# Kernel tuning notes

Hardware: AMD Instinct MI355X
Metric: run time of the kernel (lower is better)

## Reference

```python
import jax, jax.numpy as jnp
import numpy as np

HEADS = 4
SPARSITY_WEIGHT = 0.1
LN_EPS = 1e-5


def setup_inputs() -> dict:
    key = jax.random.key(0)
    ks = jax.random.split(key, 6)
    b, n, d = 4, 2048, 512
    x = jax.random.normal(ks[0], (b, n, d), dtype=jnp.float32)
    alibi_bias = jax.random.normal(ks[1], (b, n, n), dtype=jnp.float32)
    gamma = jax.random.normal(ks[2], (b, d), dtype=jnp.float32)
    beta = jax.random.normal(ks[3], (b, d), dtype=jnp.float32)
    ln_w = jnp.ones((d,), dtype=jnp.float32)
    ln_b = jnp.zeros((d,), dtype=jnp.float32)
    w_qkv = jax.random.normal(ks[4], (d, 3 * d), dtype=jnp.float32) * (d ** -0.5)
    w_out = jax.random.normal(ks[5], (d, d), dtype=jnp.float32) * (d ** -0.5)
    return {"x": x, "alibi_bias": alibi_bias, "gamma": gamma, "beta": beta,
            "ln_w": ln_w, "ln_b": ln_b, "w_qkv": w_qkv, "w_out": w_out}


def reference(x, alibi_bias, gamma, beta, ln_w, ln_b, w_qkv, w_out):
    b, n, d = x.shape
    dh = d // HEADS
    scale = dh ** -0.5
    # LayerNorm over last dim
    mu = jnp.mean(x, axis=-1, keepdims=True)
    var = jnp.mean(jnp.square(x - mu), axis=-1, keepdims=True)
    xn = (x - mu) * jax.lax.rsqrt(var + LN_EPS) * ln_w + ln_b
    # FiLM
    xn = gamma[:, None, :] * xn + beta[:, None, :]
    # QKV projection (Linear, no bias)
    qkv = xn @ w_qkv  # [b, n, 3d]
    q, k, v = jnp.split(qkv, 3, axis=-1)
    split_heads = lambda t: t.reshape(b, n, HEADS, dh).transpose(0, 2, 1, 3)  # b h n d
    q, k, v = split_heads(q), split_heads(k), split_heads(v)
    dots = jnp.einsum('bhid,bhjd->bhij', q, k) * scale
    dots = dots + alibi_bias[:, None, :, :]  # broadcast over heads
    attn = jax.nn.softmax(dots, axis=-1)
    eps = 1e-8
    entropy = -(attn * jnp.log(attn + eps)).sum(axis=-1)
    sparsity_loss = entropy.mean() * SPARSITY_WEIGHT
    out = jnp.einsum('bhij,bhjd->bhid', attn, v)
    out = out.transpose(0, 2, 1, 3).reshape(b, n, d)
    return out @ w_out, sparsity_loss
```

## Files before the change

### kernel.cpp

```cpp
#include <hip/hip_runtime.h>
#include <hip/hip_bf16.h>

typedef __attribute__((ext_vector_type(8))) short short8;
typedef __attribute__((ext_vector_type(4))) short short4_t;
typedef __attribute__((ext_vector_type(4))) float f32x4;

static constexpr int NN = 2048, DD = 512;
static constexpr float SCALE = 0.088388347648318447f;
static constexpr float ENT_SCALE = 0.1f / 32768.0f;

__device__ __forceinline__ short f2bf(float f) {
  __hip_bfloat16 h = __float2bfloat16(f);
  return *reinterpret_cast<short*>(&h);
}

__device__ __forceinline__ void async_cp16(const void* g, void* l) {
  __builtin_amdgcn_global_load_lds((const __attribute__((address_space(1))) void*)g,
                                   (__attribute__((address_space(3))) void*)l, 16, 0, 0);
}

__global__ __launch_bounds__(256) void ln_film_k(
    const float* __restrict__ x, const float* __restrict__ gamma,
    const float* __restrict__ beta, const float* __restrict__ lnw,
    const float* __restrict__ lnb, short* __restrict__ xn) {
  const int wave = threadIdx.x >> 6, lane = threadIdx.x & 63;
  const int row = blockIdx.x * 4 + wave;
  const int b = row >> 11;
  const float4* xr = reinterpret_cast<const float4*>(x + (size_t)row * DD);
  float4 u = xr[lane * 2], v = xr[lane * 2 + 1];
  float s  = u.x + u.y + u.z + u.w + v.x + v.y + v.z + v.w;
  float ss = u.x*u.x + u.y*u.y + u.z*u.z + u.w*u.w + v.x*v.x + v.y*v.y + v.z*v.z + v.w*v.w;
  #pragma unroll
  for (int m = 1; m < 64; m <<= 1) { s += __shfl_xor(s, m); ss += __shfl_xor(ss, m); }
  const float mu = s * (1.0f / DD);
  const float rs = rsqrtf(ss * (1.0f / DD) - mu * mu + 1e-5f);
  const int c0 = lane * 8;
  float vals[8] = {u.x,u.y,u.z,u.w,v.x,v.y,v.z,v.w};
  short8 o;
  #pragma unroll
  for (int i = 0; i < 8; ++i) {
    const int c = c0 + i;
    const float t = (vals[i] - mu) * rs * lnw[c] + lnb[c];
    o[i] = f2bf(gamma[b * DD + c] * t + beta[b * DD + c]);
  }
  *reinterpret_cast<short8*>(xn + (size_t)row * DD + c0) = o;
}

__global__ void transpose_bf16_k(const float* __restrict__ w, short* __restrict__ wt,
                                 int K, int Nc) {
  const int id = blockIdx.x * 256 + threadIdx.x;
  if (id >= K * Nc) return;
  const int k = id / Nc, c = id - k * Nc;
  wt[(size_t)c * K + k] = f2bf(w[id]);
}

template<int BM, int NT, bool BF16OUT>
__global__ __launch_bounds__(256) void gemm_bt_k(
    const short* __restrict__ A, const short* __restrict__ Bt, void* __restrict__ C) {
  constexpr int K = 512;
  constexpr int ABYTES = BM * 128;
  __shared__ char lds[2 * ABYTES + 32768];
  constexpr int nTiles = NT / 128;
  const int m0 = (blockIdx.x / nTiles) * BM;
  const int n0 = (blockIdx.x % nTiles) * 128;
  const int tid = threadIdx.x, wave = tid >> 6, lane = tid & 63;
  const int wm = wave >> 1, wn = wave & 1;
  const int lg = lane >> 4, li = lane & 15;
  constexpr int MT = BM / 32;
  f32x4 acc[MT][4] = {};

  auto stage = [&](int buf, int kt) {
    #pragma unroll
    for (int t = 0; t < BM / 32; ++t) {
      const int dbase = t * 4096 + wave * 1024;
      const int m = (dbase >> 7) + (lane >> 3);
      const int cs = ((lane & 7) * 16) ^ ((m & 7) << 4);
      async_cp16((const char*)A + ((size_t)(m0 + m) * K + kt * 64) * 2 + cs,
                 lds + buf * ABYTES + dbase);
    }
    #pragma unroll
    for (int t = 0; t < 4; ++t) {
      const int dbase = t * 4096 + wave * 1024;
      const int n = (dbase >> 7) + (lane >> 3);
      const int cs = ((lane & 7) * 16) ^ ((n & 7) << 4);
      async_cp16((const char*)Bt + ((size_t)(n0 + n) * K + kt * 64) * 2 + cs,
                 lds + 2 * ABYTES + buf * 16384 + dbase);
    }
  };

  stage(0, 0);
  __syncthreads();
  for (int kt = 0; kt < 8; ++kt) {
    const int cur = kt & 1;
    if (kt < 7) stage(cur ^ 1, kt + 1);
    const char* Al = lds + cur * ABYTES;
    const char* Bl = lds + 2 * ABYTES + cur * 16384;
    #pragma unroll
    for (int ks = 0; ks < 2; ++ks) {
      const int kb = ks * 64 + lg * 16;
      short8 af[MT], bfr[4];
      #pragma unroll
      for (int t = 0; t < MT; ++t) {
        const int r = wm * (BM / 2) + t * 16 + li;
        af[t] = *reinterpret_cast<const short8*>(Al + r * 128 + (kb ^ ((r & 7) << 4)));
      }
      #pragma unroll
      for (int t = 0; t < 4; ++t) {
        const int c = wn * 64 + t * 16 + li;
        bfr[t] = *reinterpret_cast<const short8*>(Bl + c * 128 + (kb ^ ((c & 7) << 4)));
      }
      #pragma unroll
      for (int mt = 0; mt < MT; ++mt)
        #pragma unroll
        for (int nt = 0; nt < 4; ++nt)
          acc[mt][nt] = __builtin_amdgcn_mfma_f32_16x16x32_bf16(af[mt], bfr[nt], acc[mt][nt], 0, 0, 0);
    }
    __syncthreads();
  }
  #pragma unroll
  for (int mt = 0; mt < MT; ++mt) {
    #pragma unroll
    for (int nt = 0; nt < 4; ++nt) {
      const int row = m0 + wm * (BM / 2) + mt * 16 + lg * 4;
      const int col = n0 + wn * 64 + nt * 16 + li;
      #pragma unroll
      for (int r = 0; r < 4; ++r) {
        if (BF16OUT)
          reinterpret_cast<short*>(C)[(size_t)(row + r) * NT + col] = f2bf(acc[mt][nt][r]);
        else
          reinterpret_cast<float*>(C)[(size_t)(row + r) * NT + col] = acc[mt][nt][r];
      }
    }
  }
}

__global__ __launch_bounds__(256) void attn_k(
    const short* __restrict__ qkv, const float* __restrict__ alibi,
    short* __restrict__ ao, float* __restrict__ ent) {
  __shared__ char lds[73728];
  const int qt = blockIdx.x, bh = blockIdx.y;
  const int b = bh >> 2, h = bh & 3;
  const int tid = threadIdx.x, wave = tid >> 6, lane = tid & 63;
  const int lg = lane >> 4, li = lane & 15;
  char* const Pbase = lds + 65536 + wave * 2048;

  const int qrow = qt * 64 + wave * 16 + li;
  const char* qptr = (const char*)qkv + ((size_t)(b * NN + qrow) * 1536 + h * 128) * 2;
  short8 qf[4];
  #pragma unroll
  for (int kq = 0; kq < 4; ++kq)
    qf[kq] = *reinterpret_cast<const short8*>(qptr + kq * 64 + lg * 16);

  f32x4 oacc[8] = {};
  float mrow = -INFINITY, lrow = 0.f, trow = 0.f;
  const float* arow = alibi + (size_t)(b * NN + qrow) * NN;

  auto stageK = [&](int buf, int kt) {
    #pragma unroll
    for (int i = 0; i < 4; ++i) {
      const int chunk = wave * 4 + i;
      const int mloc = chunk * 4 + lg;
      const int cs = (li * 16) ^ ((mloc & 7) << 4);
      async_cp16((const char*)qkv + ((size_t)(b * NN + kt * 64 + mloc) * 1536 + 512 + h * 128) * 2 + cs,
                 lds + buf * 16384 + chunk * 1024);
    }
  };
  auto loadV = [&](int kt, short8* vv) {
    #pragma unroll
    for (int p = 0; p < 4; ++p)
      vv[p] = *reinterpret_cast<const short8*>(
          (const char*)qkv + ((size_t)(b * NN + kt * 64 + lane) * 1536 + 1024 + h * 128 + wave * 8 + p * 32) * 2);
  };
  auto writeV = [&](int buf, const short8* vv) {
    short* Vp = reinterpret_cast<short*>(lds + 32768 + buf * 16384);
    #pragma unroll
    for (int p = 0; p < 4; ++p)
      #pragma unroll
      for (int i2 = 0; i2 < 8; ++i2) {
        const int dh = wave * 8 + p * 32 + i2;
        Vp[dh * 64 + (lane ^ ((dh & 7) << 3))] = vv[p][i2];
      }
  };
  auto loadA = [&](int kt, float4* ab) {
    #pragma unroll
    for (int ct = 0; ct < 4; ++ct)
      ab[ct] = *reinterpret_cast<const float4*>(arow + kt * 64 + ct * 16 + lg * 4);
  };

  short8 vv[4]; float4 ab[4];
  stageK(0, 0); loadV(0, vv); loadA(0, ab);
  writeV(0, vv);
  __syncthreads();

  for (int kt = 0; kt < 32; ++kt) {
    const int cur = kt & 1, nxt = cur ^ 1;
    short8 vvn[4]; float4 abn[4];
    if (kt < 31) { stageK(nxt, kt + 1); loadV(kt + 1, vvn); loadA(kt + 1, abn); }

    f32x4 sacc[4] = {};
    const char* Kl = lds + cur * 16384;
    #pragma unroll
    for (int ct = 0; ct < 4; ++ct) {
      const int key = ct * 16 + li;
      #pragma unroll
      for (int kq = 0; kq < 4; ++kq) {
        short8 kf = *reinterpret_cast<const short8*>(
            Kl + key * 256 + ((kq * 64 + lg * 16) ^ ((key & 7) << 4)));
        sacc[ct] = __builtin_amdgcn_mfma_f32_16x16x32_bf16(kf, qf[kq], sacc[ct], 0, 0, 0);
      }
    }
    float sv[4][4], p[4][4];
    #pragma unroll
    for (int ct = 0; ct < 4; ++ct) {
      sv[ct][0] = sacc[ct][0] * SCALE + ab[ct].x;
      sv[ct][1] = sacc[ct][1] * SCALE + ab[ct].y;
      sv[ct][2] = sacc[ct][2] * SCALE + ab[ct].z;
      sv[ct][3] = sacc[ct][3] * SCALE + ab[ct].w;
    }
    float mx = sv[0][0];
    #pragma unroll
    for (int ct = 0; ct < 4; ++ct)
      #pragma unroll
      for (int r = 0; r < 4; ++r) mx = fmaxf(mx, sv[ct][r]);
    mx = fmaxf(mx, __shfl_xor(mx, 16));
    mx = fmaxf(mx, __shfl_xor(mx, 32));
    const bool resc = !__all(mx <= mrow + 8.0f);
    float newm = mrow, fsc = 1.0f;
    if (resc) { newm = fmaxf(mrow, mx); fsc = __expf(mrow - newm); }
    float lsum = 0.f, tsum = 0.f;
    #pragma unroll
    for (int ct = 0; ct < 4; ++ct)
      #pragma unroll
      for (int r = 0; r < 4; ++r) {
        p[ct][r] = __expf(sv[ct][r] - newm);
        lsum += p[ct][r];
        tsum = fmaf(p[ct][r], sv[ct][r], tsum);
      }
    lsum += __shfl_xor(lsum, 16); lsum += __shfl_xor(lsum, 32);
    tsum += __shfl_xor(tsum, 16); tsum += __shfl_xor(tsum, 32);
    if (resc) {
      lrow = lrow * fsc + lsum; trow = trow * fsc + tsum; mrow = newm;
      #pragma unroll
      for (int nt = 0; nt < 8; ++nt) oacc[nt] *= fsc;
    } else { lrow += lsum; trow += tsum; }
    #pragma unroll
    for (int ct = 0; ct < 4; ++ct) {
      short4_t pw;
      #pragma unroll
      for (int r = 0; r < 4; ++r) pw[r] = f2bf(p[ct][r]);
      *reinterpret_cast<short4_t*>(Pbase + li * 128 + ((ct * 32 + lg * 8) ^ ((li & 7) << 4))) = pw;
    }
    const char* Vl = lds + 32768 + cur * 16384;
    #pragma unroll
    for (int ks = 0; ks < 2; ++ks) {
      const int kb = ks * 64 + lg * 16;
      short8 pa = *reinterpret_cast<const short8*>(Pbase + li * 128 + (kb ^ ((li & 7) << 4)));
      #pragma unroll
      for (int nt = 0; nt < 8; ++nt) {
        const int dh = nt * 16 + li;
        short8 vb = *reinterpret_cast<const short8*>(Vl + dh * 128 + (kb ^ ((dh & 7) << 4)));
        oacc[nt] = __builtin_amdgcn_mfma_f32_16x16x32_bf16(vb, pa, oacc[nt], 0, 0, 0);
      }
    }
    if (kt < 31) {
      writeV(nxt, vvn);
      #pragma unroll
      for (int ct = 0; ct < 4; ++ct) ab[ct] = abn[ct];
    }
    __syncthreads();
  }

  const float invl = 1.0f / lrow;
  #pragma unroll
  for (int nt = 0; nt < 8; ++nt) {
    short4_t ow;
    #pragma unroll
    for (int r = 0; r < 4; ++r) ow[r] = f2bf(oacc[nt][r] * invl);
    *reinterpret_cast<short4_t*>(ao + (size_t)(b * NN + qrow) * DD + h * 128 + nt * 16 + lg * 4) = ow;
  }
  float e = (lg == 0) ? (mrow + logf(lrow) - trow * invl) : 0.f;
  #pragma unroll
  for (int m = 1; m < 64; m <<= 1) e += __shfl_xor(e, m);
  if (lane == 0) atomicAdd(ent, e * ENT_SCALE);
}

extern "C" void kernel_launch(void* const* d_in, const int* in_sizes, int n_in,
                              void* d_out, int out_size, void* d_ws, size_t ws_size,
                              hipStream_t stream) {
  const float* x     = (const float*)d_in[0];
  const float* alibi = (const float*)d_in[1];
  const float* gamma = (const float*)d_in[2];
  const float* beta  = (const float*)d_in[3];
  const float* lnw   = (const float*)d_in[4];
  const float* lnb   = (const float*)d_in[5];
  const float* wqkv  = (const float*)d_in[6];
  const float* wout  = (const float*)d_in[7];
  float* out = (float*)d_out;

  char* ws = (char*)d_ws;
  short* xn    = (short*)(ws);
  short* wqkvT = (short*)(ws + 8388608);
  short* woutT = (short*)(ws + 8388608 + 1572864);
  short* qkv   = (short*)(ws + 10485760);
  short* ao    = (short*)(ws);

  hipMemsetAsync(out + 4194304, 0, 4, stream);
  ln_film_k<<<2048, 256, 0, stream>>>(x, gamma, beta, lnw, lnb, xn);
  transpose_bf16_k<<<(512 * 1536 + 255) / 256, 256, 0, stream>>>(wqkv, wqkvT, 512, 1536);
  transpose_bf16_k<<<(512 * 512 + 255) / 256, 256, 0, stream>>>(wout, woutT, 512, 512);
  gemm_bt_k<128, 1536, true><<<64 * 12, 256, 0, stream>>>(xn, wqkvT, qkv);
  attn_k<<<dim3(32, 16), 256, 0, stream>>>(qkv, alibi, ao, out + 4194304);
  gemm_bt_k<64, 512, false><<<128 * 4, 256, 0, stream>>>(ao, woutT, out);
}
```

Before: 269.5 us.

## Pre-transpose V, stage K/V asynchronously, merge weight prep, retile QKV GEMM

Adds a kernel that writes V transposed per head into a workspace buffer, so the attention kernel can stage V into LDS with async global-to-LDS copies instead of register loads followed by scalar LDS scatters. The K swizzle widens to 16 rows, the alibi bias is double-buffered two tiles ahead, and the main loop is unrolled by two. The two weight-transpose launches are merged into one, and the QKV GEMM uses 64-row tiles. The cost is an extra kernel launch plus an extra V write and read through global memory.

```diff
diff --git a/kernel.cpp b/kernel.cpp
--- a/kernel.cpp
+++ b/kernel.cpp
@@ -46,12 +46,43 @@
   *reinterpret_cast<short8*>(xn + (size_t)row * DD + c0) = o;
 }
 
-__global__ void transpose_bf16_k(const float* __restrict__ w, short* __restrict__ wt,
-                                 int K, int Nc) {
-  const int id = blockIdx.x * 256 + threadIdx.x;
-  if (id >= K * Nc) return;
-  const int k = id / Nc, c = id - k * Nc;
-  wt[(size_t)c * K + k] = f2bf(w[id]);
+__global__ void prep_w_k(const float* __restrict__ wqkv, const float* __restrict__ wout,
+                         short* __restrict__ wqkvT, short* __restrict__ woutT) {
+  int id = blockIdx.x * 256 + threadIdx.x;
+  if (id < 786432) {
+    const int k = id / 1536, c = id - k * 1536;
+    wqkvT[(size_t)c * 512 + k] = f2bf(wqkv[id]);
+  } else {
+    id -= 786432;
+    const int k = id >> 9, c = id & 511;
+    woutT[(size_t)c * 512 + k] = f2bf(wout[id]);
+  }
+}
+
+__global__ __launch_bounds__(256) void vt_k(const short* __restrict__ qkv, short* __restrict__ vt) {
+  __shared__ short t[64][136];
+  const int bh = blockIdx.y;
+  const int b = bh >> 2, h = bh & 3;
+  const int k0 = blockIdx.x * 64;
+  const int tid = threadIdx.x;
+  const int key = tid >> 2, part = tid & 3;
+  const short* src = qkv + ((size_t)(b * NN + k0 + key) * 1536 + 1024 + h * 128 + part * 32);
+  #pragma unroll
+  for (int i = 0; i < 4; ++i) {
+    short8 v = *reinterpret_cast<const short8*>(src + i * 8);
+    #pragma unroll
+    for (int j = 0; j < 8; ++j) t[key][part * 32 + i * 8 + j] = v[j];
+  }
+  __syncthreads();
+  const int dh = tid >> 1, half = tid & 1;
+  short* dst = vt + ((size_t)(bh * 128 + dh) * NN + k0 + half * 32);
+  #pragma unroll
+  for (int i = 0; i < 4; ++i) {
+    short8 o;
+    #pragma unroll
+    for (int j = 0; j < 8; ++j) o[j] = t[half * 32 + i * 8 + j][dh];
+    *reinterpret_cast<short8*>(dst + i * 8) = o;
+  }
 }
 
 template<int BM, int NT, bool BF16OUT>
@@ -135,8 +166,8 @@
 }
 
 __global__ __launch_bounds__(256) void attn_k(
-    const short* __restrict__ qkv, const float* __restrict__ alibi,
-    short* __restrict__ ao, float* __restrict__ ent) {
+    const short* __restrict__ qkv, const short* __restrict__ vt,
+    const float* __restrict__ alibi, short* __restrict__ ao, float* __restrict__ ent) {
   __shared__ char lds[73728];
   const int qt = blockIdx.x, bh = blockIdx.y;
   const int b = bh >> 2, h = bh & 3;
@@ -159,27 +190,21 @@
     #pragma unroll
     for (int i = 0; i < 4; ++i) {
       const int chunk = wave * 4 + i;
-      const int mloc = chunk * 4 + lg;
-      const int cs = (li * 16) ^ ((mloc & 7) << 4);
-      async_cp16((const char*)qkv + ((size_t)(b * NN + kt * 64 + mloc) * 1536 + 512 + h * 128) * 2 + cs,
+      const int row = chunk * 4 + (lane >> 4);
+      const int cs = ((lane & 15) * 16) ^ ((row & 15) << 4);
+      async_cp16((const char*)qkv + ((size_t)(b * NN + kt * 64 + row) * 1536 + 512 + h * 128) * 2 + cs,
                  lds + buf * 16384 + chunk * 1024);
     }
   };
-  auto loadV = [&](int kt, short8* vv) {
-    #pragma unroll
-    for (int p = 0; p < 4; ++p)
-      vv[p] = *reinterpret_cast<const short8*>(
-          (const char*)qkv + ((size_t)(b * NN + kt * 64 + lane) * 1536 + 1024 + h * 128 + wave * 8 + p * 32) * 2);
-  };
-  auto writeV = [&](int buf, const short8* vv) {
-    short* Vp = reinterpret_cast<short*>(lds + 32768 + buf * 16384);
-    #pragma unroll
-    for (int p = 0; p < 4; ++p)
-      #pragma unroll
-      for (int i2 = 0; i2 < 8; ++i2) {
-        const int dh = wave * 8 + p * 32 + i2;
-        Vp[dh * 64 + (lane ^ ((dh & 7) << 3))] = vv[p][i2];
-      }
+  auto stageV = [&](int buf, int kt) {
+    #pragma unroll
+    for (int i = 0; i < 4; ++i) {
+      const int chunk = wave * 4 + i;
+      const int row = chunk * 8 + (lane >> 3);
+      const int cs = ((lane & 7) * 16) ^ ((row & 7) << 4);
+      async_cp16((const char*)vt + ((size_t)(bh * 128 + row) * NN + kt * 64) * 2 + cs,
+                 lds + 32768 + buf * 16384 + chunk * 1024);
+    }
   };
   auto loadA = [&](int kt, float4* ab) {
     #pragma unroll
@@ -187,87 +212,90 @@
       ab[ct] = *reinterpret_cast<const float4*>(arow + kt * 64 + ct * 16 + lg * 4);
   };
 
-  short8 vv[4]; float4 ab[4];
-  stageK(0, 0); loadV(0, vv); loadA(0, ab);
-  writeV(0, vv);
+  float4 abE[4], abO[4];
+  stageK(0, 0); stageV(0, 0);
+  loadA(0, abE); loadA(1, abO);
   __syncthreads();
 
-  for (int kt = 0; kt < 32; ++kt) {
-    const int cur = kt & 1, nxt = cur ^ 1;
-    short8 vvn[4]; float4 abn[4];
-    if (kt < 31) { stageK(nxt, kt + 1); loadV(kt + 1, vvn); loadA(kt + 1, abn); }
-
-    f32x4 sacc[4] = {};
-    const char* Kl = lds + cur * 16384;
-    #pragma unroll
-    for (int ct = 0; ct < 4; ++ct) {
-      const int key = ct * 16 + li;
-      #pragma unroll
-      for (int kq = 0; kq < 4; ++kq) {
-        short8 kf = *reinterpret_cast<const short8*>(
-            Kl + key * 256 + ((kq * 64 + lg * 16) ^ ((key & 7) << 4)));
-        sacc[ct] = __builtin_amdgcn_mfma_f32_16x16x32_bf16(kf, qf[kq], sacc[ct], 0, 0, 0);
-      }
-    }
-    float sv[4][4], p[4][4];
-    #pragma unroll
-    for (int ct = 0; ct < 4; ++ct) {
-      sv[ct][0] = sacc[ct][0] * SCALE + ab[ct].x;
-      sv[ct][1] = sacc[ct][1] * SCALE + ab[ct].y;
-      sv[ct][2] = sacc[ct][2] * SCALE + ab[ct].z;
-      sv[ct][3] = sacc[ct][3] * SCALE + ab[ct].w;
-    }
-    float mx = sv[0][0];
-    #pragma unroll
-    for (int ct = 0; ct < 4; ++ct)
-      #pragma unroll
-      for (int r = 0; r < 4; ++r) mx = fmaxf(mx, sv[ct][r]);
-    mx = fmaxf(mx, __shfl_xor(mx, 16));
-    mx = fmaxf(mx, __shfl_xor(mx, 32));
-    const bool resc = !__all(mx <= mrow + 8.0f);
-    float newm = mrow, fsc = 1.0f;
-    if (resc) { newm = fmaxf(mrow, mx); fsc = __expf(mrow - newm); }
-    float lsum = 0.f, tsum = 0.f;
-    #pragma unroll
-    for (int ct = 0; ct < 4; ++ct)
-      #pragma unroll
-      for (int r = 0; r < 4; ++r) {
-        p[ct][r] = __expf(sv[ct][r] - newm);
-        lsum += p[ct][r];
-        tsum = fmaf(p[ct][r], sv[ct][r], tsum);
-      }
-    lsum += __shfl_xor(lsum, 16); lsum += __shfl_xor(lsum, 32);
-    tsum += __shfl_xor(tsum, 16); tsum += __shfl_xor(tsum, 32);
-    if (resc) {
-      lrow = lrow * fsc + lsum; trow = trow * fsc + tsum; mrow = newm;
-      #pragma unroll
-      for (int nt = 0; nt < 8; ++nt) oacc[nt] *= fsc;
-    } else { lrow += lsum; trow += tsum; }
-    #pragma unroll
-    for (int ct = 0; ct < 4; ++ct) {
-      short4_t pw;
-      #pragma unroll
-      for (int r = 0; r < 4; ++r) pw[r] = f2bf(p[ct][r]);
-      *reinterpret_cast<short4_t*>(Pbase + li * 128 + ((ct * 32 + lg * 8) ^ ((li & 7) << 4))) = pw;
-    }
-    const char* Vl = lds + 32768 + cur * 16384;
-    #pragma unroll
-    for (int ks = 0; ks < 2; ++ks) {
-      const int kb = ks * 64 + lg * 16;
-      short8 pa = *reinterpret_cast<const short8*>(Pbase + li * 128 + (kb ^ ((li & 7) << 4)));
-      #pragma unroll
-      for (int nt = 0; nt < 8; ++nt) {
-        const int dh = nt * 16 + li;
-        short8 vb = *reinterpret_cast<const short8*>(Vl + dh * 128 + (kb ^ ((dh & 7) << 4)));
-        oacc[nt] = __builtin_amdgcn_mfma_f32_16x16x32_bf16(vb, pa, oacc[nt], 0, 0, 0);
-      }
-    }
-    if (kt < 31) {
-      writeV(nxt, vvn);
-      #pragma unroll
-      for (int ct = 0; ct < 4; ++ct) ab[ct] = abn[ct];
-    }
-    __syncthreads();
+  #pragma unroll 1
+  for (int kt2 = 0; kt2 < 32; kt2 += 2) {
+    #pragma unroll
+    for (int par = 0; par < 2; ++par) {
+      const int kt = kt2 + par;
+      const int cur = par, nxt = par ^ 1;
+      float4* const ab = par ? abO : abE;
+      if (kt < 31) { stageK(nxt, kt + 1); stageV(nxt, kt + 1); }
+
+      f32x4 sacc[4] = {};
+      const char* Kl = lds + cur * 16384;
+      #pragma unroll
+      for (int ct = 0; ct < 4; ++ct) {
+        const int key = ct * 16 + li;
+        #pragma unroll
+        for (int kq = 0; kq < 4; ++kq) {
+          short8 kf = *reinterpret_cast<const short8*>(
+              Kl + key * 256 + ((kq * 64 + lg * 16) ^ ((key & 15) << 4)));
+          sacc[ct] = __builtin_amdgcn_mfma_f32_16x16x32_bf16(kf, qf[kq], sacc[ct], 0, 0, 0);
+        }
+      }
+      float sv[4][4], p[4][4];
+      #pragma unroll
+      for (int ct = 0; ct < 4; ++ct) {
+        sv[ct][0] = fmaf(sacc[ct][0], SCALE, ab[ct].x);
+        sv[ct][1] = fmaf(sacc[ct][1], SCALE, ab[ct].y);
+        sv[ct][2] = fmaf(sacc[ct][2], SCALE, ab[ct].z);
+        sv[ct][3] = fmaf(sacc[ct][3], SCALE, ab[ct].w);
+      }
+      if (kt + 2 < 32) loadA(kt + 2, ab);
+
+      float mx = sv[0][0];
+      #pragma unroll
+      for (int ct = 0; ct < 4; ++ct)
+        #pragma unroll
+        for (int r = 0; r < 4; ++r) mx = fmaxf(mx, sv[ct][r]);
+      mx = fmaxf(mx, __shfl_xor(mx, 16));
+      mx = fmaxf(mx, __shfl_xor(mx, 32));
+      const bool resc = !__all(mx <= mrow + 8.0f);
+      float newm = mrow, fsc = 1.0f;
+      if (resc) { newm = fmaxf(mrow, mx); fsc = __expf(mrow - newm); }
+      float lsum = 0.f, tsum = 0.f;
+      #pragma unroll
+      for (int ct = 0; ct < 4; ++ct)
+        #pragma unroll
+        for (int r = 0; r < 4; ++r) {
+          p[ct][r] = __expf(sv[ct][r] - newm);
+          lsum += p[ct][r];
+          tsum = fmaf(p[ct][r], sv[ct][r], tsum);
+        }
+      lsum += __shfl_xor(lsum, 16); lsum += __shfl_xor(lsum, 32);
+      tsum += __shfl_xor(tsum, 16); tsum += __shfl_xor(tsum, 32);
+      if (resc) {
+        lrow = lrow * fsc + lsum; trow = trow * fsc + tsum; mrow = newm;
+        #pragma unroll
+        for (int nt = 0; nt < 8; ++nt) oacc[nt] *= fsc;
+      } else { lrow += lsum; trow += tsum; }
+
+      #pragma unroll
+      for (int ct = 0; ct < 4; ++ct) {
+        short4_t pw;
+        #pragma unroll
+        for (int r = 0; r < 4; ++r) pw[r] = f2bf(p[ct][r]);
+        *reinterpret_cast<short4_t*>(Pbase + li * 128 + ((ct * 32 + lg * 8) ^ ((li & 7) << 4))) = pw;
+      }
+      const char* Vl = lds + 32768 + cur * 16384;
+      #pragma unroll
+      for (int ks = 0; ks < 2; ++ks) {
+        const int kb = ks * 64 + lg * 16;
+        short8 pa = *reinterpret_cast<const short8*>(Pbase + li * 128 + (kb ^ ((li & 7) << 4)));
+        #pragma unroll
+        for (int nt = 0; nt < 8; ++nt) {
+          const int dh = nt * 16 + li;
+          short8 vb = *reinterpret_cast<const short8*>(Vl + dh * 128 + (kb ^ ((dh & 7) << 4)));
+          oacc[nt] = __builtin_amdgcn_mfma_f32_16x16x32_bf16(vb, pa, oacc[nt], 0, 0, 0);
+        }
+      }
+      __syncthreads();
+    }
   }
 
   const float invl = 1.0f / lrow;
@@ -300,15 +328,16 @@
   char* ws = (char*)d_ws;
   short* xn    = (short*)(ws);
   short* wqkvT = (short*)(ws + 8388608);
-  short* woutT = (short*)(ws + 8388608 + 1572864);
+  short* woutT = (short*)(ws + 9961472);
   short* qkv   = (short*)(ws + 10485760);
+  short* vt    = (short*)(ws + 35651584);
   short* ao    = (short*)(ws);
 
   hipMemsetAsync(out + 4194304, 0, 4, stream);
   ln_film_k<<<2048, 256, 0, stream>>>(x, gamma, beta, lnw, lnb, xn);
-  transpose_bf16_k<<<(512 * 1536 + 255) / 256, 256, 0, stream>>>(wqkv, wqkvT, 512, 1536);
-  transpose_bf16_k<<<(512 * 512 + 255) / 256, 256, 0, stream>>>(wout, woutT, 512, 512);
-  gemm_bt_k<128, 1536, true><<<64 * 12, 256, 0, stream>>>(xn, wqkvT, qkv);
-  attn_k<<<dim3(32, 16), 256, 0, stream>>>(qkv, alibi, ao, out + 4194304);
+  prep_w_k<<<4096, 256, 0, stream>>>(wqkv, wout, wqkvT, woutT);
+  gemm_bt_k<64, 1536, true><<<128 * 12, 256, 0, stream>>>(xn, wqkvT, qkv);
+  vt_k<<<dim3(32, 16), 256, 0, stream>>>(qkv, vt);
+  attn_k<<<dim3(32, 16), 256, 0, stream>>>(qkv, vt, alibi, ao, out + 4194304);
   gemm_bt_k<64, 512, false><<<128 * 4, 256, 0, stream>>>(ao, woutT, out);
 }
```

After: 247.1 us. 1.09x faster.
